# Optimization experiments

Measured on AMD Instinct MI355X. Metric: run time of the kernel, lower is better.

Reference implementation:

```python
import jax, jax.numpy as jnp
import numpy as np

# ---- model hyperparams (match init_kwargs / Mamba1 defaults) ----
SEQ_LEN, PRED_LEN, PATCH, STRIDE = 512, 96, 16, 16
D_MODEL, N_LAYER, N_VARS = 128, 2, 32
D_INNER, D_STATE, D_CONV, DT_RANK = 2 * D_MODEL, 16, 4, 8  # d_inner=2*d_model, dt_rank=ceil(d_model/16)
BATCH = 16
EPS = 1e-5


def setup_inputs() -> dict:
    key = jax.random.key(0)
    ks = jax.random.split(key, 20)
    s = 0.02
    inp = {
        'x_enc': jax.random.normal(ks[0], (BATCH, SEQ_LEN, N_VARS), jnp.float32),
        'x_mark_enc': jax.random.normal(ks[1], (BATCH, SEQ_LEN, 4), jnp.float32),
        'x_dec': jax.random.normal(ks[2], (BATCH, PRED_LEN, N_VARS), jnp.float32),
        'x_mark_dec': jax.random.normal(ks[3], (BATCH, PRED_LEN, 4), jnp.float32),
        # patch embedding: Linear(patch_len -> d_model, bias=False)
        'patch_w': jax.random.normal(ks[4], (D_MODEL, PATCH), jnp.float32) * s,
        # per-layer Mamba1 params, stacked on leading layer axis
        'norm_w': jnp.ones((N_LAYER, D_MODEL), jnp.float32),
        'in_proj_w': jax.random.normal(ks[5], (N_LAYER, 2 * D_INNER, D_MODEL), jnp.float32) * s,
        'conv_w': jax.random.normal(ks[6], (N_LAYER, D_INNER, D_CONV), jnp.float32) * s,
        'conv_b': jnp.zeros((N_LAYER, D_INNER), jnp.float32),
        'x_proj_w': jax.random.normal(ks[7], (N_LAYER, DT_RANK + 2 * D_STATE, D_INNER), jnp.float32) * s,
        'dt_proj_w': jax.random.normal(ks[8], (N_LAYER, D_INNER, DT_RANK), jnp.float32) * s,
        'dt_proj_b': jax.random.normal(ks[9], (N_LAYER, D_INNER), jnp.float32) * 0.1 - 4.0,  # softplus -> small dt
        'A_log': jnp.tile(jnp.log(jnp.arange(1, D_STATE + 1, dtype=jnp.float32))[None, None, :], (N_LAYER, D_INNER, 1)),
        'D_skip': jnp.ones((N_LAYER, D_INNER), jnp.float32),
        'out_proj_w': jax.random.normal(ks[10], (N_LAYER, D_MODEL, D_INNER), jnp.float32) * s,
        'final_norm_w': jnp.ones((D_MODEL,), jnp.float32),
        # head: Linear(d_model*seq_len//patch_len -> pred_len)
        'head_w': jax.random.normal(ks[11], (PRED_LEN, D_MODEL * SEQ_LEN // PATCH), jnp.float32) * s,
        'head_b': jnp.zeros((PRED_LEN,), jnp.float32),
    }
    return inp


def rmsnorm(x, w):
    return x * jax.lax.rsqrt(jnp.mean(x * x, axis=-1, keepdims=True) + EPS) * w


def selective_scan(u, dt, A, Bm, Cm, Dp):
    # u, dt: (B,L,Di); Bm, Cm: (B,L,N); A: (Di,N); Dp: (Di,)
    def step(h, inp):
        dt_t, B_t, C_t, u_t = inp  # (B,Di),(B,N),(B,N),(B,Di)
        dA = jnp.exp(dt_t[:, :, None] * A)                      # (B,Di,N)
        h = dA * h + dt_t[:, :, None] * B_t[:, None, :] * u_t[:, :, None]
        y = jnp.einsum('bdn,bn->bd', h, C_t)
        return h, y

    B_, L, Di = u.shape
    h0 = jnp.zeros((B_, Di, A.shape[1]), u.dtype)
    xs = (dt.transpose(1, 0, 2), Bm.transpose(1, 0, 2), Cm.transpose(1, 0, 2), u.transpose(1, 0, 2))
    _, ys = jax.lax.scan(step, h0, xs)
    return ys.transpose(1, 0, 2) + u * Dp  # skip connection D*u


def mamba_mixer(x, in_w, cw, cb, xp_w, dt_w, dt_b, A_log, Dp, out_w):
    # x: (B,L,d_model)
    xz = x @ in_w.T                                   # (B,L,2*Di)
    xs_, z = jnp.split(xz, 2, axis=-1)
    xc = xs_.transpose(0, 2, 1)                       # (B,Di,L)
    xc = jax.lax.conv_general_dilated(
        xc, cw[:, None, :], (1,), [(D_CONV - 1, 0)],  # causal depthwise conv
        dimension_numbers=('NCH', 'OIH', 'NCH'), feature_group_count=D_INNER)
    xc = jax.nn.silu(xc + cb[None, :, None])
    u = xc.transpose(0, 2, 1)                         # (B,L,Di)
    x_dbl = u @ xp_w.T                                # (B,L,dt_rank+2N)
    dt, Bm, Cm = jnp.split(x_dbl, [DT_RANK, DT_RANK + D_STATE], axis=-1)
    dt = jax.nn.softplus(dt @ dt_w.T + dt_b)          # (B,L,Di)
    A = -jnp.exp(A_log)                               # (Di,N)
    y = selective_scan(u, dt, A, Bm, Cm, Dp)
    y = y * jax.nn.silu(z)
    return y @ out_w.T


def reference(x_enc, x_mark_enc, x_dec, x_mark_dec, patch_w, norm_w, in_proj_w,
              conv_w, conv_b, x_proj_w, dt_proj_w, dt_proj_b, A_log, D_skip,
              out_proj_w, final_norm_w, head_w, head_b):
    b, _, c = x_enc.shape
    # instance norm over time (stats detached)
    means = jax.lax.stop_gradient(jnp.mean(x_enc, axis=1, keepdims=True))
    xe = x_enc - means
    stdev = jax.lax.stop_gradient(jnp.sqrt(jnp.var(xe, axis=1, keepdims=True) + EPS))
    xe = xe / stdev
    # patching: stride == patch_len so unfold == reshape
    xp = xe.transpose(0, 2, 1).reshape(b, c, SEQ_LEN // PATCH, PATCH)  # (b,c,l,patch)
    enc = jnp.einsum('bclp,dp->bcld', xp, patch_w).reshape(b, c * (SEQ_LEN // PATCH), D_MODEL)
    # Mamba encoder: pre-norm residual blocks + final norm
    x = enc
    for i in range(N_LAYER):
        h = rmsnorm(x, norm_w[i])
        x = x + mamba_mixer(h, in_proj_w[i], conv_w[i], conv_b[i], x_proj_w[i],
                            dt_proj_w[i], dt_proj_b[i], A_log[i], D_skip[i], out_proj_w[i])
    x = rmsnorm(x, final_norm_w)
    # prediction head: b (c l) d -> (b c) (l d) -> linear -> (b, pred, c)
    l = SEQ_LEN // PATCH
    xh = x.reshape(b, c, l * D_MODEL)
    out = xh @ head_w.T + head_b                      # (b,c,pred)
    dec_out = out.transpose(0, 2, 1)                  # (b,pred,c)
    dec_out = dec_out * stdev[:, :1, :] + means[:, :1, :]
    return dec_out
```

## Files before the change

### kernel.cpp

```cpp
#include <hip/hip_runtime.h>
#include <hip/hip_bf16.h>
#include <math.h>

#define BATCH   16
#define SEQL    512
#define NVARS   32
#define PATCHL  16
#define LTOK    32
#define DMODEL  128
#define NLAYER  2
#define DIN     256
#define DSTATE  16
#define DTRANK  8
#define DCONV   4
#define PRED    96
#define TOK     1024
#define NTOK    (BATCH*TOK)
#define EPSF    1e-5f
#define NCH     64
#define CHL     16

typedef __attribute__((ext_vector_type(8))) short bf16x8;
typedef __attribute__((ext_vector_type(4))) float f32x4;
typedef __hip_bfloat16 bf16;

__global__ __launch_bounds__(256) void k_cast(
    const float* __restrict__ a, const float* __restrict__ b,
    const float* __restrict__ c, const float* __restrict__ d,
    int na, int nb, int nc, int nd, bf16* __restrict__ out,
    const float* __restrict__ A_log, float* __restrict__ a1s, int* __restrict__ pwf,
    float* __restrict__ hg)
{
    int i = blockIdx.x * 256 + threadIdx.x;
    int total = na + nb + nc + nd;
    if (i < total) {
        float v;
        if (i < na) v = a[i];
        else if (i < na + nb) v = b[i - na];
        else if (i < na + nb + nc) v = c[i - na - nb];
        else v = d[i - na - nb - nc];
        out[i] = __float2bfloat16(v);
    } else if (i < total + NLAYER * DIN) {
        int j = i - total;
        const float* al = A_log + (size_t)j * DSTATE;
        float a1 = -__expf(al[0]);
        bool pw = true;
        #pragma unroll
        for (int n = 1; n < 16; n++) {
            float av = -__expf(al[n]);
            pw = pw && (fabsf(av - (n + 1) * a1) <= 1e-5f * fabsf((n + 1) * a1));
        }
        a1s[j] = a1;
        pwf[j] = pw ? 1 : 0;
    } else if (i < total + NLAYER * DIN + 512 * PRED) {
        hg[i - total - NLAYER * DIN] = 0.f;
    }
}

__global__ __launch_bounds__(256) void k_instnorm_patch(
    const float* __restrict__ x_enc, const float* __restrict__ patch_w,
    float* __restrict__ x, float* __restrict__ means, float* __restrict__ stdev)
{
    int bc = blockIdx.x;
    int b = bc >> 5, c = bc & 31;
    __shared__ float xe[SEQL];
    __shared__ float pw[DMODEL * PATCHL];
    __shared__ float red[8];
    int tid = threadIdx.x;

    float v0 = x_enc[((size_t)b * SEQL + tid) * NVARS + c];
    float v1 = x_enc[((size_t)b * SEQL + tid + 256) * NVARS + c];
    for (int i = tid; i < DMODEL * PATCHL; i += 256) pw[i] = patch_w[i];

    float s = v0 + v1;
    for (int o = 1; o < 64; o <<= 1) s += __shfl_xor(s, o, 64);
    if ((tid & 63) == 0) red[tid >> 6] = s;
    __syncthreads();
    float mean = (red[0] + red[1] + red[2] + red[3]) * (1.f / 512.f);

    float d0 = v0 - mean, d1 = v1 - mean;
    float q = d0 * d0 + d1 * d1;
    for (int o = 1; o < 64; o <<= 1) q += __shfl_xor(q, o, 64);
    if ((tid & 63) == 0) red[4 + (tid >> 6)] = q;
    __syncthreads();
    float var = (red[4] + red[5] + red[6] + red[7]) * (1.f / 512.f);
    float sd = sqrtf(var + EPSF);
    float rsd = 1.f / sd;
    if (tid == 0) { means[bc] = mean; stdev[bc] = sd; }

    xe[tid] = d0 * rsd;
    xe[tid + 256] = d1 * rsd;
    __syncthreads();

    size_t base = ((size_t)b * TOK + (size_t)c * LTOK) * DMODEL;
    for (int o = tid; o < LTOK * DMODEL; o += 256) {
        int l = o >> 7, dm = o & 127;
        float acc = 0.f;
        #pragma unroll
        for (int p = 0; p < PATCHL; p++) acc += xe[l * PATCHL + p] * pw[dm * PATCHL + p];
        x[base + o] = acc;
    }
}

__global__ __launch_bounds__(256) void k_rmsnorm(
    const float* __restrict__ in, const float* __restrict__ w,
    bf16* __restrict__ out)
{
    int wave = threadIdx.x >> 6, lane = threadIdx.x & 63;
    int tok = blockIdx.x * 4 + wave;
    const float* r = in + (size_t)tok * DMODEL;
    float a = r[lane], bv = r[lane + 64];
    float q = a * a + bv * bv;
    for (int o = 1; o < 64; o <<= 1) q += __shfl_xor(q, o, 64);
    float rms = rsqrtf(q * (1.f / DMODEL) + EPSF);
    bf16* o_ = out + (size_t)tok * DMODEL;
    o_[lane]      = __float2bfloat16(a  * rms * w[lane]);
    o_[lane + 64] = __float2bfloat16(bv * rms * w[lane + 64]);
}

template <int MODE>
__global__ __launch_bounds__(256) void mfma_gemm(
    const bf16* __restrict__ A, const bf16* __restrict__ W,
    float* __restrict__ C, bf16* __restrict__ C2, bf16* __restrict__ C3,
    int M, int N, int K, int lda, int kper)
{
    __shared__ ushort Asm[128][40];
    __shared__ ushort Wsm[128][40];
    int bm = blockIdx.y * 128, bn = blockIdx.x * 128;
    int tid = threadIdx.x;
    int w = tid >> 6, l = tid & 63;
    int wr = w >> 1, wc = w & 1;
    int kb = (l >> 4) * 8, lr = l & 15;

    f32x4 acc[4][4];
    #pragma unroll
    for (int i = 0; i < 4; i++)
        #pragma unroll
        for (int j = 0; j < 4; j++) acc[i][j] = (f32x4){0.f, 0.f, 0.f, 0.f};

    int kbeg = blockIdx.z * kper;
    for (int k0 = kbeg; k0 < kbeg + kper; k0 += 32) {
        #pragma unroll
        for (int i = 0; i < 2; i++) {
            int idx = tid + 256 * i;
            int row = idx >> 2, kq = (idx & 3) * 8;
            *(float4*)&Asm[row][kq] =
                *(const float4*)&A[(size_t)(bm + row) * lda + k0 + kq];
            float4 wv = make_float4(0.f, 0.f, 0.f, 0.f);
            if (bn + row < N)
                wv = *(const float4*)&W[(size_t)(bn + row) * K + k0 + kq];
            *(float4*)&Wsm[row][kq] = wv;
        }
        __syncthreads();
        bf16x8 af[4], bfr[4];
        #pragma unroll
        for (int f = 0; f < 4; f++) {
            af[f]  = *(const bf16x8*)&Asm[wr * 64 + f * 16 + lr][kb];
            bfr[f] = *(const bf16x8*)&Wsm[wc * 64 + f * 16 + lr][kb];
        }
        #pragma unroll
        for (int mf = 0; mf < 4; mf++)
            #pragma unroll
            for (int nf = 0; nf < 4; nf++)
                acc[mf][nf] = __builtin_amdgcn_mfma_f32_16x16x32_bf16(
                    af[mf], bfr[nf], acc[mf][nf], 0, 0, 0);
        __syncthreads();
    }

    int rbase = bm + wr * 64 + (l >> 4) * 4;
    int cbase = bn + wc * 64 + lr;
    #pragma unroll
    for (int mf = 0; mf < 4; mf++) {
        #pragma unroll
        for (int nf = 0; nf < 4; nf++) {
            int n = cbase + nf * 16;
            if (n >= N) continue;
            #pragma unroll
            for (int r = 0; r < 4; r++) {
                int m = rbase + mf * 16 + r;
                float v = acc[mf][nf][r];
                if (MODE == 0) C[(size_t)m * N + n] = v;
                else if (MODE == 2) atomicAdd(&C[(size_t)m * N + n], v);
                else {
                    if (n < 256) C3[(size_t)m * 256 + n] = __float2bfloat16(v);
                    else C2[(size_t)m * 256 + (n - 256)] = __float2bfloat16(v);
                }
            }
        }
    }
}

__device__ __forceinline__ float softplus_f(float x) {
    return (x > 8.f) ? x : __logf(1.f + __expf(x));
}

__global__ __launch_bounds__(256) void k_convx1(
    const bf16* __restrict__ xs, const float* __restrict__ cw,
    const float* __restrict__ cb, const bf16* __restrict__ xw,
    const float* __restrict__ dtw, const float* __restrict__ dtb_,
    const float* __restrict__ a1s, const int* __restrict__ pwf,
    const float* __restrict__ A_log,
    bf16* __restrict__ ubf, float* __restrict__ xdbl,
    float* __restrict__ q, float* __restrict__ sdt_out)
{
    int blk = blockIdx.x;
    int b = blk >> 6, ch = blk & (NCH - 1);
    int d = threadIdx.x;
    __shared__ ushort u_lds[16][264];
    __shared__ float xdbl_lds[16][40];

    float c0 = cw[d * 4], c1 = cw[d * 4 + 1], c2 = cw[d * 4 + 2], c3 = cw[d * 4 + 3];
    float cbias = cb[d];
    int tloc0 = ch * CHL;
    const bf16* col = xs + ((size_t)b * TOK + tloc0) * 256 + d;
    float xv[19];
    #pragma unroll
    for (int i = 0; i < 19; i++) {
        int tg = tloc0 - 3 + i;
        xv[i] = (tg >= 0) ? __bfloat162float(col[(size_t)(i - 3) * 256]) : 0.f;
    }
    bf16* uout = ubf + ((size_t)b * TOK + tloc0) * 256 + d;
    #pragma unroll
    for (int t = 0; t < 16; t++) {
        float a = cbias + xv[t] * c0 + xv[t + 1] * c1 + xv[t + 2] * c2 + xv[t + 3] * c3;
        float s = __fdividef(a, 1.f + __expf(-a));
        bf16 ub = __float2bfloat16(s);
        u_lds[t][d] = *(ushort*)&ub;
        uout[(size_t)t * 256] = ub;
    }
    __syncthreads();

    int w = d >> 6, l = d & 63;
    if (w < 3) {
        int lr = l & 15, kb = (l >> 4) * 8;
        int nrow = w * 16 + lr;
        bool valid = nrow < 40;
        const bf16* wrow = xw + (size_t)nrow * 256;
        f32x4 acc = (f32x4){0.f, 0.f, 0.f, 0.f};
        #pragma unroll
        for (int ks = 0; ks < 8; ks++) {
            bf16x8 af = *(const bf16x8*)&u_lds[lr][ks * 32 + kb];
            bf16x8 bfr = (bf16x8){0, 0, 0, 0, 0, 0, 0, 0};
            if (valid) bfr = *(const bf16x8*)&wrow[ks * 32 + kb];
            acc = __builtin_amdgcn_mfma_f32_16x16x32_bf16(af, bfr, acc, 0, 0, 0);
        }
        int ncol = w * 16 + (l & 15);
        if (ncol < 40) {
            #pragma unroll
            for (int r = 0; r < 4; r++) {
                int t = (l >> 4) * 4 + r;
                xdbl_lds[t][ncol] = acc[r];
                xdbl[((size_t)b * TOK + tloc0 + t) * 40 + ncol] = acc[r];
            }
        }
    }
    __syncthreads();

    float a1 = a1s[d];
    bool pw = pwf[d] != 0;
    float w8[8];
    #pragma unroll
    for (int j = 0; j < 8; j++) w8[j] = dtw[d * 8 + j];
    float bias = dtb_[d];
    float h[16];
    #pragma unroll
    for (int n = 0; n < 16; n++) h[n] = 0.f;
    float sdt = 0.f;

    if (pw) {
        for (int t = 0; t < CHL; t++) {
            float acc = bias;
            #pragma unroll
            for (int j = 0; j < 8; j++) acc += xdbl_lds[t][j] * w8[j];
            float dtv = softplus_f(acc);
            ushort uraw = u_lds[t][d];
            float uu = __bfloat162float(*(bf16*)&uraw);
            sdt += dtv;
            float du = dtv * uu;
            float dA[16];
            dA[0] = __expf(dtv * a1);
            #pragma unroll
            for (int n = 1; n < 16; n++) dA[n] = dA[(n - 1) >> 1] * dA[n >> 1];
            #pragma unroll
            for (int n = 0; n < 16; n++)
                h[n] = dA[n] * h[n] + du * xdbl_lds[t][8 + n];
        }
    } else {
        float Av[16];
        #pragma unroll
        for (int n = 0; n < 16; n++) Av[n] = -__expf(A_log[d * 16 + n]);
        for (int t = 0; t < CHL; t++) {
            float acc = bias;
            #pragma unroll
            for (int j = 0; j < 8; j++) acc += xdbl_lds[t][j] * w8[j];
            float dtv = softplus_f(acc);
            ushort uraw = u_lds[t][d];
            float uu = __bfloat162float(*(bf16*)&uraw);
            sdt += dtv;
            float du = dtv * uu;
            #pragma unroll
            for (int n = 0; n < 16; n++)
                h[n] = __expf(dtv * Av[n]) * h[n] + du * xdbl_lds[t][8 + n];
        }
    }
    float* qp = q + ((size_t)blk * 16) * 256 + d;
    #pragma unroll
    for (int n = 0; n < 16; n++) qp[(size_t)n * 256] = h[n];
    sdt_out[(size_t)blk * 256 + d] = sdt;
}

__global__ __launch_bounds__(256) void k_scan2(
    const float* __restrict__ A_log, const float* __restrict__ sdt_in,
    float* __restrict__ q)
{
    int idx = blockIdx.x * 256 + threadIdx.x;
    int d = idx & 255, n = (idx >> 8) & 15, b = idx >> 12;
    float Av = -__expf(A_log[d * 16 + n]);
    float h = 0.f;
    for (int g = 0; g < NCH / 8; g++) {
        float qv[8], sv[8];
        #pragma unroll
        for (int j = 0; j < 8; j++) {
            size_t blk = (size_t)b * NCH + g * 8 + j;
            qv[j] = q[(blk * 16 + n) * 256 + d];
            sv[j] = sdt_in[blk * 256 + d];
        }
        #pragma unroll
        for (int j = 0; j < 8; j++) {
            size_t blk = (size_t)b * NCH + g * 8 + j;
            float P = __expf(Av * sv[j]);
            q[(blk * 16 + n) * 256 + d] = h;
            h = P * h + qv[j];
        }
    }
}

__global__ __launch_bounds__(256) void k_scan3o(
    const bf16* __restrict__ ubf, const float* __restrict__ xdbl,
    const float* __restrict__ dtw, const float* __restrict__ dtb_,
    const float* __restrict__ a1s, const int* __restrict__ pwf,
    const float* __restrict__ A_log, const float* __restrict__ Dp,
    const float* __restrict__ q, const bf16* __restrict__ zbf,
    const bf16* __restrict__ ow, float* __restrict__ x)
{
    int blk = blockIdx.x;
    int b = blk >> 6, ch = blk & (NCH - 1);
    int d = threadIdx.x;
    __shared__ ushort y_lds[16][264];

    float a1 = a1s[d];
    bool pw = pwf[d] != 0;
    float w8[8];
    #pragma unroll
    for (int j = 0; j < 8; j++) w8[j] = dtw[d * 8 + j];
    float bias = dtb_[d];
    float Dv = Dp[d];
    float h[16];
    const float* qp = q + ((size_t)blk * 16) * 256 + d;
    #pragma unroll
    for (int n = 0; n < 16; n++) h[n] = qp[(size_t)n * 256];

    size_t tok0 = (size_t)b * TOK + ch * CHL;
    const float* row = xdbl + tok0 * 40;
    const bf16* up = ubf + tok0 * 256 + d;
    const bf16* zp = zbf + tok0 * 256 + d;

    if (pw) {
        for (int t = 0; t < CHL; t++, row += 40, up += 256, zp += 256) {
            float acc = bias;
            #pragma unroll
            for (int j = 0; j < 8; j++) acc += row[j] * w8[j];
            float dtv = softplus_f(acc);
            float uu = __bfloat162float(*up);
            float du = dtv * uu;
            float dA[16];
            dA[0] = __expf(dtv * a1);
            #pragma unroll
            for (int n = 1; n < 16; n++) dA[n] = dA[(n - 1) >> 1] * dA[n >> 1];
            float ya = 0.f;
            #pragma unroll
            for (int n = 0; n < 16; n++) {
                h[n] = dA[n] * h[n] + du * row[8 + n];
                ya += h[n] * row[24 + n];
            }
            float zv = __bfloat162float(*zp);
            float sz = __fdividef(zv, 1.f + __expf(-zv));
            bf16 yb = __float2bfloat16((ya + uu * Dv) * sz);
            y_lds[t][d] = *(ushort*)&yb;
        }
    } else {
        float Av[16];
        #pragma unroll
        for (int n = 0; n < 16; n++) Av[n] = -__expf(A_log[d * 16 + n]);
        for (int t = 0; t < CHL; t++, row += 40, up += 256, zp += 256) {
            float acc = bias;
            #pragma unroll
            for (int j = 0; j < 8; j++) acc += row[j] * w8[j];
            float dtv = softplus_f(acc);
            float uu = __bfloat162float(*up);
            float du = dtv * uu;
            float ya = 0.f;
            #pragma unroll
            for (int n = 0; n < 16; n++) {
                h[n] = __expf(dtv * Av[n]) * h[n] + du * row[8 + n];
                ya += h[n] * row[24 + n];
            }
            float zv = __bfloat162float(*zp);
            float sz = __fdividef(zv, 1.f + __expf(-zv));
            bf16 yb = __float2bfloat16((ya + uu * Dv) * sz);
            y_lds[t][d] = *(ushort*)&yb;
        }
    }
    __syncthreads();

    int w = d >> 6, l = d & 63;
    int lr = l & 15, kb = (l >> 4) * 8;
    const bf16* wr0 = ow + (size_t)(w * 32 + lr) * 256;
    const bf16* wr1 = ow + (size_t)(w * 32 + 16 + lr) * 256;
    f32x4 acc0 = (f32x4){0.f, 0.f, 0.f, 0.f};
    f32x4 acc1 = (f32x4){0.f, 0.f, 0.f, 0.f};
    #pragma unroll
    for (int ks = 0; ks < 8; ks++) {
        bf16x8 af = *(const bf16x8*)&y_lds[lr][ks * 32 + kb];
        bf16x8 b0 = *(const bf16x8*)&wr0[ks * 32 + kb];
        bf16x8 b1 = *(const bf16x8*)&wr1[ks * 32 + kb];
        acc0 = __builtin_amdgcn_mfma_f32_16x16x32_bf16(af, b0, acc0, 0, 0, 0);
        acc1 = __builtin_amdgcn_mfma_f32_16x16x32_bf16(af, b1, acc1, 0, 0, 0);
    }
    int trow = (l >> 4) * 4;
    float* xp = x + (tok0 + trow) * (size_t)DMODEL;
    #pragma unroll
    for (int r = 0; r < 4; r++) {
        xp[(size_t)r * DMODEL + w * 32 + lr]      += acc0[r];
        xp[(size_t)r * DMODEL + w * 32 + 16 + lr] += acc1[r];
    }
}

__global__ __launch_bounds__(256) void k_head_ep(
    const float* __restrict__ hg, const float* __restrict__ hb,
    const float* __restrict__ means, const float* __restrict__ stdev,
    float* __restrict__ out)
{
    int i = blockIdx.x * 256 + threadIdx.x;
    if (i >= BATCH * PRED * NVARS) return;
    int c = i & 31;
    int p = (i >> 5) % PRED;
    int b = i / (PRED * NVARS);
    float v = hg[((size_t)b * NVARS + c) * PRED + p] + hb[p];
    out[i] = v * stdev[b * NVARS + c] + means[b * NVARS + c];
}

extern "C" void kernel_launch(void* const* d_in, const int* in_sizes, int n_in,
                              void* d_out, int out_size, void* d_ws, size_t ws_size,
                              hipStream_t stream)
{
    const float* x_enc   = (const float*)d_in[0];
    const float* patch_w = (const float*)d_in[4];
    const float* norm_w  = (const float*)d_in[5];
    const float* in_w    = (const float*)d_in[6];
    const float* conv_w  = (const float*)d_in[7];
    const float* conv_b  = (const float*)d_in[8];
    const float* xp_w    = (const float*)d_in[9];
    const float* dt_w    = (const float*)d_in[10];
    const float* dt_b    = (const float*)d_in[11];
    const float* A_log   = (const float*)d_in[12];
    const float* D_skip  = (const float*)d_in[13];
    const float* out_w   = (const float*)d_in[14];
    const float* fnorm_w = (const float*)d_in[15];
    const float* head_w  = (const float*)d_in[16];
    const float* head_b  = (const float*)d_in[17];
    float* out = (float*)d_out;

    float* ws    = (float*)d_ws;
    float* means = ws;
    float* stdv  = ws + 512;
    float* x     = ws + 1024;
    float* xdbl  = x    + (size_t)NTOK * 128;
    float* qbuf  = xdbl + (size_t)NTOK * 40;
    float* sbuf  = qbuf + (size_t)BATCH * NCH * DIN * DSTATE;
    float* hg    = sbuf + (size_t)BATCH * NCH * DIN;
    float* a1s   = hg + 512 * PRED;
    int*   pwf   = (int*)(a1s + NLAYER * DIN);
    bf16* hbf  = (bf16*)(pwf + NLAYER * DIN);
    bf16* xsbf = hbf + (size_t)NTOK * 128;
    bf16* zbf  = xsbf + (size_t)NTOK * 256;
    bf16* ubf  = zbf + (size_t)NTOK * 256;
    bf16* wbf  = ubf + (size_t)NTOK * 256;

    const int NIW = NLAYER * 2 * DIN * DMODEL;
    const int NXW = NLAYER * (DTRANK + 2*DSTATE) * DIN;
    const int NOW = NLAYER * DMODEL * DIN;
    const int NHW = PRED * LTOK * DMODEL;
    bf16* iwbf = wbf;
    bf16* xwbf = iwbf + NIW;
    bf16* owbf = xwbf + NXW;
    bf16* hwbf = owbf + NOW;

    int castN = NIW + NXW + NOW + NHW + NLAYER * DIN + 512 * PRED;
    k_cast<<<(castN + 255) / 256, 256, 0, stream>>>(
        in_w, xp_w, out_w, head_w, NIW, NXW, NOW, NHW, wbf, A_log, a1s, pwf, hg);

    k_instnorm_patch<<<BATCH * NVARS, 256, 0, stream>>>(x_enc, patch_w, x, means, stdv);

    for (int layer = 0; layer < NLAYER; layer++) {
        const float* nw  = norm_w + layer * DMODEL;
        const float* cw  = conv_w + layer * DIN * DCONV;
        const float* cb  = conv_b + layer * DIN;
        const float* dw  = dt_w   + layer * DIN * DTRANK;
        const float* db  = dt_b   + layer * DIN;
        const float* al  = A_log  + layer * DIN * DSTATE;
        const float* dp  = D_skip + layer * DIN;
        const float* a1l = a1s + layer * DIN;
        const int*   pwl = pwf + layer * DIN;
        const bf16* iw = iwbf + (size_t)layer * 2 * DIN * DMODEL;
        const bf16* xw = xwbf + (size_t)layer * (DTRANK + 2 * DSTATE) * DIN;
        const bf16* ow = owbf + (size_t)layer * DMODEL * DIN;

        k_rmsnorm<<<NTOK / 4, 256, 0, stream>>>(x, nw, hbf);
        mfma_gemm<3><<<dim3(4, NTOK / 128, 1), 256, 0, stream>>>(
            hbf, iw, nullptr, zbf, xsbf, NTOK, 512, DMODEL, DMODEL, DMODEL);
        k_convx1<<<BATCH * NCH, 256, 0, stream>>>(
            xsbf, cw, cb, xw, dw, db, a1l, pwl, al, ubf, xdbl, qbuf, sbuf);
        k_scan2<<<(BATCH * DIN * DSTATE) / 256, 256, 0, stream>>>(al, sbuf, qbuf);
        k_scan3o<<<BATCH * NCH, 256, 0, stream>>>(
            ubf, xdbl, dw, db, a1l, pwl, al, dp, qbuf, zbf, ow, x);
    }

    k_rmsnorm<<<NTOK / 4, 256, 0, stream>>>(x, fnorm_w, hbf);
    mfma_gemm<2><<<dim3(1, 4, 32), 256, 0, stream>>>(
        hbf, hwbf, hg, nullptr, nullptr, 512, PRED, LTOK * DMODEL, LTOK * DMODEL, 128);
    k_head_ep<<<(BATCH * PRED * NVARS + 255) / 256, 256, 0, stream>>>(
        hg, head_b, means, stdv, out);
}
```

Measured before the change: 172.3 us.

## Fuse RMSNorm into patch-embed and scan epilogue; store chunk states in bf16

Removes the standalone RMSNorm kernels by computing the pre-norm (and final norm) inside the patch-embedding kernel and the scan/out-projection epilogue, using LDS to gather full token rows before writing bf16 normalized activations. Also switches the inter-chunk state buffer used by the three scan kernels from fp32 to bf16, halving its memory traffic. This saves three launches and a full read of the residual stream per layer, at the cost of extra LDS and a syncthreads in those kernels and reduced precision in the carried scan states.

```diff
diff --git a/kernel.cpp b/kernel.cpp
--- a/kernel.cpp
+++ b/kernel.cpp
@@ -59,13 +59,16 @@
 
 __global__ __launch_bounds__(256) void k_instnorm_patch(
     const float* __restrict__ x_enc, const float* __restrict__ patch_w,
-    float* __restrict__ x, float* __restrict__ means, float* __restrict__ stdev)
+    const float* __restrict__ nw0,
+    float* __restrict__ x, bf16* __restrict__ hbf,
+    float* __restrict__ means, float* __restrict__ stdev)
 {
     int bc = blockIdx.x;
     int b = bc >> 5, c = bc & 31;
     __shared__ float xe[SEQL];
     __shared__ float pw[DMODEL * PATCHL];
     __shared__ float red[8];
+    __shared__ float enc_lds[LTOK][DMODEL];
     int tid = threadIdx.x;
 
     float v0 = x_enc[((size_t)b * SEQL + tid) * NVARS + c];
@@ -99,23 +102,23 @@
         #pragma unroll
         for (int p = 0; p < PATCHL; p++) acc += xe[l * PATCHL + p] * pw[dm * PATCHL + p];
         x[base + o] = acc;
-    }
-}
-
-__global__ __launch_bounds__(256) void k_rmsnorm(
-    const float* __restrict__ in, const float* __restrict__ w,
-    bf16* __restrict__ out)
-{
-    int wave = threadIdx.x >> 6, lane = threadIdx.x & 63;
-    int tok = blockIdx.x * 4 + wave;
-    const float* r = in + (size_t)tok * DMODEL;
-    float a = r[lane], bv = r[lane + 64];
-    float q = a * a + bv * bv;
-    for (int o = 1; o < 64; o <<= 1) q += __shfl_xor(q, o, 64);
-    float rms = rsqrtf(q * (1.f / DMODEL) + EPSF);
-    bf16* o_ = out + (size_t)tok * DMODEL;
-    o_[lane]      = __float2bfloat16(a  * rms * w[lane]);
-    o_[lane + 64] = __float2bfloat16(bv * rms * w[lane + 64]);
+        enc_lds[l][dm] = acc;
+    }
+    __syncthreads();
+
+    int t = tid >> 3, g = tid & 7;
+    float vals[16];
+    float ss = 0.f;
+    #pragma unroll
+    for (int j = 0; j < 16; j++) { vals[j] = enc_lds[t][g * 16 + j]; ss += vals[j] * vals[j]; }
+    ss += __shfl_xor(ss, 1, 64);
+    ss += __shfl_xor(ss, 2, 64);
+    ss += __shfl_xor(ss, 4, 64);
+    float rms = rsqrtf(ss * (1.f / DMODEL) + EPSF);
+    bf16* hp = hbf + (base + (size_t)t * DMODEL);
+    #pragma unroll
+    for (int j = 0; j < 16; j++)
+        hp[g * 16 + j] = __float2bfloat16(vals[j] * rms * nw0[g * 16 + j]);
 }
 
 template <int MODE>
@@ -179,8 +182,7 @@
             for (int r = 0; r < 4; r++) {
                 int m = rbase + mf * 16 + r;
                 float v = acc[mf][nf][r];
-                if (MODE == 0) C[(size_t)m * N + n] = v;
-                else if (MODE == 2) atomicAdd(&C[(size_t)m * N + n], v);
+                if (MODE == 2) atomicAdd(&C[(size_t)m * N + n], v);
                 else {
                     if (n < 256) C3[(size_t)m * 256 + n] = __float2bfloat16(v);
                     else C2[(size_t)m * 256 + (n - 256)] = __float2bfloat16(v);
@@ -201,7 +203,7 @@
     const float* __restrict__ a1s, const int* __restrict__ pwf,
     const float* __restrict__ A_log,
     bf16* __restrict__ ubf, float* __restrict__ xdbl,
-    float* __restrict__ q, float* __restrict__ sdt_out)
+    bf16* __restrict__ q, float* __restrict__ sdt_out)
 {
     int blk = blockIdx.x;
     int b = blk >> 6, ch = blk & (NCH - 1);
@@ -303,15 +305,15 @@
                 h[n] = __expf(dtv * Av[n]) * h[n] + du * xdbl_lds[t][8 + n];
         }
     }
-    float* qp = q + ((size_t)blk * 16) * 256 + d;
-    #pragma unroll
-    for (int n = 0; n < 16; n++) qp[(size_t)n * 256] = h[n];
+    bf16* qp = q + ((size_t)blk * 16) * 256 + d;
+    #pragma unroll
+    for (int n = 0; n < 16; n++) qp[(size_t)n * 256] = __float2bfloat16(h[n]);
     sdt_out[(size_t)blk * 256 + d] = sdt;
 }
 
 __global__ __launch_bounds__(256) void k_scan2(
     const float* __restrict__ A_log, const float* __restrict__ sdt_in,
-    float* __restrict__ q)
+    bf16* __restrict__ q)
 {
     int idx = blockIdx.x * 256 + threadIdx.x;
     int d = idx & 255, n = (idx >> 8) & 15, b = idx >> 12;
@@ -322,14 +324,14 @@
         #pragma unroll
         for (int j = 0; j < 8; j++) {
             size_t blk = (size_t)b * NCH + g * 8 + j;
-            qv[j] = q[(blk * 16 + n) * 256 + d];
+            qv[j] = __bfloat162float(q[(blk * 16 + n) * 256 + d]);
             sv[j] = sdt_in[blk * 256 + d];
         }
         #pragma unroll
         for (int j = 0; j < 8; j++) {
             size_t blk = (size_t)b * NCH + g * 8 + j;
             float P = __expf(Av * sv[j]);
-            q[(blk * 16 + n) * 256 + d] = h;
+            q[(blk * 16 + n) * 256 + d] = __float2bfloat16(h);
             h = P * h + qv[j];
         }
     }
@@ -340,13 +342,15 @@
     const float* __restrict__ dtw, const float* __restrict__ dtb_,
     const float* __restrict__ a1s, const int* __restrict__ pwf,
     const float* __restrict__ A_log, const float* __restrict__ Dp,
-    const float* __restrict__ q, const bf16* __restrict__ zbf,
-    const bf16* __restrict__ ow, float* __restrict__ x)
+    const bf16* __restrict__ q, const bf16* __restrict__ zbf,
+    const bf16* __restrict__ ow, const float* __restrict__ nwn,
+    float* __restrict__ x, bf16* __restrict__ hout)
 {
     int blk = blockIdx.x;
     int b = blk >> 6, ch = blk & (NCH - 1);
     int d = threadIdx.x;
     __shared__ ushort y_lds[16][264];
+    __shared__ float xn_lds[16][132];
 
     float a1 = a1s[d];
     bool pw = pwf[d] != 0;
@@ -356,9 +360,9 @@
     float bias = dtb_[d];
     float Dv = Dp[d];
     float h[16];
-    const float* qp = q + ((size_t)blk * 16) * 256 + d;
-    #pragma unroll
-    for (int n = 0; n < 16; n++) h[n] = qp[(size_t)n * 256];
+    const bf16* qp = q + ((size_t)blk * 16) * 256 + d;
+    #pragma unroll
+    for (int n = 0; n < 16; n++) h[n] = __bfloat162float(qp[(size_t)n * 256]);
 
     size_t tok0 = (size_t)b * TOK + ch * CHL;
     const float* row = xdbl + tok0 * 40;
@@ -431,9 +435,29 @@
     float* xp = x + (tok0 + trow) * (size_t)DMODEL;
     #pragma unroll
     for (int r = 0; r < 4; r++) {
-        xp[(size_t)r * DMODEL + w * 32 + lr]      += acc0[r];
-        xp[(size_t)r * DMODEL + w * 32 + 16 + lr] += acc1[r];
-    }
+        float v0 = xp[(size_t)r * DMODEL + w * 32 + lr] + acc0[r];
+        float v1 = xp[(size_t)r * DMODEL + w * 32 + 16 + lr] + acc1[r];
+        xp[(size_t)r * DMODEL + w * 32 + lr] = v0;
+        xp[(size_t)r * DMODEL + w * 32 + 16 + lr] = v1;
+        xn_lds[trow + r][w * 32 + lr] = v0;
+        xn_lds[trow + r][w * 32 + 16 + lr] = v1;
+    }
+    __syncthreads();
+
+    int t = d >> 4, g = d & 15;
+    float vals[8];
+    float ss = 0.f;
+    #pragma unroll
+    for (int j = 0; j < 8; j++) { vals[j] = xn_lds[t][g * 8 + j]; ss += vals[j] * vals[j]; }
+    ss += __shfl_xor(ss, 1, 64);
+    ss += __shfl_xor(ss, 2, 64);
+    ss += __shfl_xor(ss, 4, 64);
+    ss += __shfl_xor(ss, 8, 64);
+    float rms = rsqrtf(ss * (1.f / DMODEL) + EPSF);
+    bf16* hp = hout + (tok0 + t) * (size_t)DMODEL;
+    #pragma unroll
+    for (int j = 0; j < 8; j++)
+        hp[g * 8 + j] = __float2bfloat16(vals[j] * rms * nwn[g * 8 + j]);
 }
 
 __global__ __launch_bounds__(256) void k_head_ep(
@@ -476,8 +500,7 @@
     float* stdv  = ws + 512;
     float* x     = ws + 1024;
     float* xdbl  = x    + (size_t)NTOK * 128;
-    float* qbuf  = xdbl + (size_t)NTOK * 40;
-    float* sbuf  = qbuf + (size_t)BATCH * NCH * DIN * DSTATE;
+    float* sbuf  = xdbl + (size_t)NTOK * 40;
     float* hg    = sbuf + (size_t)BATCH * NCH * DIN;
     float* a1s   = hg + 512 * PRED;
     int*   pwf   = (int*)(a1s + NLAYER * DIN);
@@ -485,7 +508,8 @@
     bf16* xsbf = hbf + (size_t)NTOK * 128;
     bf16* zbf  = xsbf + (size_t)NTOK * 256;
     bf16* ubf  = zbf + (size_t)NTOK * 256;
-    bf16* wbf  = ubf + (size_t)NTOK * 256;
+    bf16* qbuf = ubf + (size_t)NTOK * 256;
+    bf16* wbf  = qbuf + (size_t)BATCH * NCH * DSTATE * DIN;
 
     const int NIW = NLAYER * 2 * DIN * DMODEL;
     const int NXW = NLAYER * (DTRANK + 2*DSTATE) * DIN;
@@ -500,10 +524,10 @@
     k_cast<<<(castN + 255) / 256, 256, 0, stream>>>(
         in_w, xp_w, out_w, head_w, NIW, NXW, NOW, NHW, wbf, A_log, a1s, pwf, hg);
 
-    k_instnorm_patch<<<BATCH * NVARS, 256, 0, stream>>>(x_enc, patch_w, x, means, stdv);
+    k_instnorm_patch<<<BATCH * NVARS, 256, 0, stream>>>(
+        x_enc, patch_w, norm_w, x, hbf, means, stdv);
 
     for (int layer = 0; layer < NLAYER; layer++) {
-        const float* nw  = norm_w + layer * DMODEL;
         const float* cw  = conv_w + layer * DIN * DCONV;
         const float* cb  = conv_b + layer * DIN;
         const float* dw  = dt_w   + layer * DIN * DTRANK;
@@ -515,18 +539,17 @@
         const bf16* iw = iwbf + (size_t)layer * 2 * DIN * DMODEL;
         const bf16* xw = xwbf + (size_t)layer * (DTRANK + 2 * DSTATE) * DIN;
         const bf16* ow = owbf + (size_t)layer * DMODEL * DIN;
-
-        k_rmsnorm<<<NTOK / 4, 256, 0, stream>>>(x, nw, hbf);
+        const float* nwn = (layer + 1 < NLAYER) ? (norm_w + (layer + 1) * DMODEL) : fnorm_w;
+
         mfma_gemm<3><<<dim3(4, NTOK / 128, 1), 256, 0, stream>>>(
             hbf, iw, nullptr, zbf, xsbf, NTOK, 512, DMODEL, DMODEL, DMODEL);
         k_convx1<<<BATCH * NCH, 256, 0, stream>>>(
             xsbf, cw, cb, xw, dw, db, a1l, pwl, al, ubf, xdbl, qbuf, sbuf);
         k_scan2<<<(BATCH * DIN * DSTATE) / 256, 256, 0, stream>>>(al, sbuf, qbuf);
         k_scan3o<<<BATCH * NCH, 256, 0, stream>>>(
-            ubf, xdbl, dw, db, a1l, pwl, al, dp, qbuf, zbf, ow, x);
-    }
-
-    k_rmsnorm<<<NTOK / 4, 256, 0, stream>>>(x, fnorm_w, hbf);
+            ubf, xdbl, dw, db, a1l, pwl, al, dp, qbuf, zbf, ow, nwn, x, hbf);
+    }
+
     mfma_gemm<2><<<dim3(1, 4, 32), 256, 0, stream>>>(
         hbf, hwbf, hg, nullptr, nullptr, 512, PRED, LTOK * DMODEL, LTOK * DMODEL, 128);
     k_head_ep<<<(BATCH * PRED * NVARS + 255) / 256, 256, 0, stream>>>(
```

Result: faster. 156.4 us (-9.2%).
